# Kernel tuning notes

Hardware: AMD Instinct MI355X
Metric: run time of the kernel (lower is better)

The kernel has to match this reference:

```python
import jax, jax.numpy as jnp
import numpy as np
import math

D_HEAD = 64
EPS = 1e-6


def _rms_norm(x, scale, eps):
    # compute in float32 like the torch reference (promote_types with float32)
    xf = x.astype(jnp.float32)
    ms = jnp.mean(xf * xf, axis=-1, keepdims=True)
    return (xf * (scale.astype(jnp.float32) * jax.lax.rsqrt(ms + eps))).astype(x.dtype)


def _apply_rotary(x, cos, sin):
    # rotate first 2*cos_dim channels, pass the rest through
    ro = cos.shape[-1] * 2
    xr, xp = x[..., :ro], x[..., ro:]
    c = jnp.concatenate([cos, cos], axis=-1)
    s = jnp.concatenate([sin, sin], axis=-1)
    x1, x2 = jnp.split(xr, 2, axis=-1)
    rot = jnp.concatenate([-x2, x1], axis=-1)
    return jnp.concatenate([xr * c + rot * s, xp], axis=-1)


def _nb_idx(L, k):
    # NATTEN neighborhood start: window of size k clamped inside [0, L)
    i = jnp.arange(L)
    start = jnp.clip(i - k // 2, 0, L - k)
    return start[:, None] + jnp.arange(k)[None, :]  # [L, k]


def setup_inputs() -> dict:
    key = jax.random.key(0)
    ks = jax.random.split(key, 6)
    n, H, W, d_model, cond_features = 2, 48, 48, 256, 256
    x = jax.random.normal(ks[0], (n, H, W, d_model), dtype=jnp.float32)
    axis = jnp.linspace(-1.0, 1.0, H, dtype=jnp.float32)
    gh, gw = jnp.meshgrid(axis, axis, indexing='ij')
    pos = jnp.stack([gh, gw], axis=-1)  # [H, W, 2]
    cond = jax.random.normal(ks[1], (n, cond_features), dtype=jnp.float32)
    w_norm = jax.random.normal(ks[2], (d_model, cond_features), dtype=jnp.float32) * 0.01
    w_qkv = jax.random.normal(ks[3], (3 * d_model, d_model), dtype=jnp.float32) / math.sqrt(d_model)
    w_out = jax.random.normal(ks[4], (d_model, d_model), dtype=jnp.float32) * 0.02
    return {"x": x, "pos": pos, "cond": cond, "w_norm": w_norm, "w_qkv": w_qkv,
            "w_out": w_out, "kernel_size": 7}


def reference(x, pos, cond, w_norm, w_qkv, w_out, kernel_size):
    n, H, W, d_model = x.shape
    e = D_HEAD
    nh = d_model // e
    k = kernel_size
    skip = x

    # AdaRMSNorm: scale = linear(cond) + 1, broadcast over h, w
    scale = (cond @ w_norm.T)[:, None, None, :] + 1.0  # [n,1,1,d_model]
    xn = _rms_norm(x, scale, EPS)

    # QKV projection -> [3, n, nh, H, W, e]
    qkv = (xn @ w_qkv.T).reshape(n, H, W, 3, nh, e)
    qkv = jnp.transpose(qkv, (3, 0, 4, 1, 2, 5))
    q, kk, v = qkv[0], qkv[1], qkv[2]

    # Axial RoPE: freqs buffer of AxialRoPE(d_head // 2)
    dim = e // 2
    nf = dim // 4
    freqs = jnp.exp(jnp.linspace(math.log(math.pi), math.log(10.0 * math.pi), nf + 1)[:-1]).astype(jnp.float32)
    fh = pos[..., 0:1] * freqs  # [H,W,nf]
    fw = pos[..., 1:2] * freqs
    fr = jnp.concatenate([fh, fw], axis=-1)  # [H,W,2*nf] == [H,W,e//4]
    cos, sin = jnp.cos(fr), jnp.sin(fr)
    q = _apply_rotary(q, cos, sin)
    kk = _apply_rotary(kk, cos, sin)
    q = q / math.sqrt(e)

    # 2D neighborhood attention (natten2dqk / natten2dav, dilation 1)
    idx_h = _nb_idx(H, k)  # [H,k]
    idx_w = _nb_idx(W, k)  # [W,k]
    kg = kk[:, :, idx_h][:, :, :, :, idx_w]  # [n,nh,H,k,W,k,e]
    vg = v[:, :, idx_h][:, :, :, :, idx_w]   # [n,nh,H,k,W,k,e]
    qk = jnp.einsum('bmije,bmipjqe->bmijpq', q, kg).reshape(n, nh, H, W, k * k)
    a = jax.nn.softmax(qk, axis=-1).reshape(n, nh, H, W, k, k)
    o = jnp.einsum('bmijpq,bmipjqe->bmije', a, vg)  # [n,nh,H,W,e]

    o = jnp.transpose(o, (0, 2, 3, 1, 4)).reshape(n, H, W, d_model)
    return o @ w_out.T + skip
```

## Files before the change

### kernel.cpp

```cpp
#include <hip/hip_runtime.h>
#include <math.h>

#define N_B 2
#define HH 48
#define WW 48
#define DM 256
#define NH 4
#define EH 64
#define KS 7
#define NPIX (N_B*HH*WW)

typedef _Float16 half8 __attribute__((ext_vector_type(8)));
typedef _Float16 half4v __attribute__((ext_vector_type(4)));
typedef float float4v __attribute__((ext_vector_type(4)));

__global__ void scale_kernel(const float* __restrict__ cond,
                             const float* __restrict__ w_norm,
                             float* __restrict__ scale) {
    int b = blockIdx.x;
    int t = threadIdx.x, wave = t >> 6, lane = t & 63;
    int d = blockIdx.y*32 + wave*8 + (lane >> 3);
    int l8 = lane & 7;
    const float4* wr4 = (const float4*)(w_norm + (size_t)d*DM) + l8*8;
    const float4* c4  = (const float4*)(cond + (size_t)b*DM) + l8*8;
    float acc = 0.f;
    #pragma unroll
    for (int j = 0; j < 8; ++j) {
        float4 w = wr4[j], c = c4[j];
        acc += w.x*c.x + w.y*c.y + w.z*c.z + w.w*c.w;
    }
    acc += __shfl_xor(acc, 1, 64);
    acc += __shfl_xor(acc, 2, 64);
    acc += __shfl_xor(acc, 4, 64);
    if (l8 == 0) scale[b*DM + d] = acc + 1.0f;
}

__global__ __launch_bounds__(256) void gemm_qkv_fused(const float* __restrict__ x,
                                                      const float* __restrict__ scale,
                                                      const float* __restrict__ B,
                                                      const float* __restrict__ pos,
                                                      _Float16* __restrict__ qh,
                                                      _Float16* __restrict__ kh,
                                                      _Float16* __restrict__ vh) {
    const int LDA = 264, LDB = 40;
    __shared__ _Float16 As[64*LDA];
    __shared__ _Float16 Bs[2][128*LDB];
    int t = threadIdx.x;
    int wave = t >> 6, lane = t & 63;
    int m0 = blockIdx.x*64;
    int n0 = blockIdx.y*128;
    int b  = m0 / (HH*WW);

    {
        int tr = t >> 2, c4 = t & 3;
        const float4* xr = (const float4*)(x + (size_t)(m0 + tr)*DM);
        float4 xv[16];
        float ss = 0.f;
        #pragma unroll
        for (int j = 0; j < 16; ++j) {
            xv[j] = xr[c4 + j*4];
            ss += xv[j].x*xv[j].x + xv[j].y*xv[j].y + xv[j].z*xv[j].z + xv[j].w*xv[j].w;
        }
        ss += __shfl_xor(ss, 1, 64);
        ss += __shfl_xor(ss, 2, 64);
        float r = rsqrtf(ss*(1.0f/DM) + 1e-6f);
        const float* sc = scale + b*DM;
        #pragma unroll
        for (int j = 0; j < 16; ++j) {
            int c = (c4 + j*4)*4;
            float4 s4 = *(const float4*)(sc + c);
            half4v h;
            h[0] = (_Float16)(xv[j].x * s4.x * r);
            h[1] = (_Float16)(xv[j].y * s4.y * r);
            h[2] = (_Float16)(xv[j].z * s4.z * r);
            h[3] = (_Float16)(xv[j].w * s4.w * r);
            *(half4v*)&As[tr*LDA + c] = h;
        }
    }
    int br = t >> 1, kk = (t & 1)*16;
    {
        const float* bp = B + (size_t)(n0 + br)*DM + kk;
        float4 b0 = ((const float4*)bp)[0], b1 = ((const float4*)bp)[1];
        float4 b2 = ((const float4*)bp)[2], b3 = ((const float4*)bp)[3];
        half8 h0, h1;
        h0[0]=(_Float16)b0.x; h0[1]=(_Float16)b0.y; h0[2]=(_Float16)b0.z; h0[3]=(_Float16)b0.w;
        h0[4]=(_Float16)b1.x; h0[5]=(_Float16)b1.y; h0[6]=(_Float16)b1.z; h0[7]=(_Float16)b1.w;
        h1[0]=(_Float16)b2.x; h1[1]=(_Float16)b2.y; h1[2]=(_Float16)b2.z; h1[3]=(_Float16)b2.w;
        h1[4]=(_Float16)b3.x; h1[5]=(_Float16)b3.y; h1[6]=(_Float16)b3.z; h1[7]=(_Float16)b3.w;
        *(half8*)&Bs[0][br*LDB + kk]     = h0;
        *(half8*)&Bs[0][br*LDB + kk + 8] = h1;
    }
    __syncthreads();

    float4v acc[2][4];
    #pragma unroll
    for (int mi = 0; mi < 2; ++mi)
        #pragma unroll
        for (int ni = 0; ni < 4; ++ni) acc[mi][ni] = (float4v){0.f,0.f,0.f,0.f};

    int frow = lane & 15, kq = (lane >> 4)*8;
    int wm = wave >> 1, wn = wave & 1;

    for (int it = 0; it < 8; ++it) {
        int cur = it & 1;
        float4 nb0, nb1, nb2, nb3;
        if (it < 7) {
            const float* bp = B + (size_t)(n0 + br)*DM + (it + 1)*32 + kk;
            nb0 = ((const float4*)bp)[0]; nb1 = ((const float4*)bp)[1];
            nb2 = ((const float4*)bp)[2]; nb3 = ((const float4*)bp)[3];
        }
        int ka = it*32 + kq;
        half8 af0 = *(const half8*)&As[(wm*32 +  0 + frow)*LDA + ka];
        half8 af1 = *(const half8*)&As[(wm*32 + 16 + frow)*LDA + ka];
        #pragma unroll
        for (int ni = 0; ni < 4; ++ni) {
            half8 bf = *(const half8*)&Bs[cur][(wn*64 + ni*16 + frow)*LDB + kq];
            acc[0][ni] = __builtin_amdgcn_mfma_f32_16x16x32_f16(af0, bf, acc[0][ni], 0, 0, 0);
            acc[1][ni] = __builtin_amdgcn_mfma_f32_16x16x32_f16(af1, bf, acc[1][ni], 0, 0, 0);
        }
        if (it < 7) {
            half8 h0, h1;
            h0[0]=(_Float16)nb0.x; h0[1]=(_Float16)nb0.y; h0[2]=(_Float16)nb0.z; h0[3]=(_Float16)nb0.w;
            h0[4]=(_Float16)nb1.x; h0[5]=(_Float16)nb1.y; h0[6]=(_Float16)nb1.z; h0[7]=(_Float16)nb1.w;
            h1[0]=(_Float16)nb2.x; h1[1]=(_Float16)nb2.y; h1[2]=(_Float16)nb2.z; h1[3]=(_Float16)nb2.w;
            h1[4]=(_Float16)nb3.x; h1[5]=(_Float16)nb3.y; h1[6]=(_Float16)nb3.z; h1[7]=(_Float16)nb3.w;
            *(half8*)&Bs[cur^1][br*LDB + kk]     = h0;
            *(half8*)&Bs[cur^1][br*LDB + kk + 8] = h1;
            __syncthreads();
        }
    }

    int sel  = blockIdx.y >> 1;
    int head = (blockIdx.y & 1)*2 + wn;
    _Float16* outp = (sel == 0) ? qh : (sel == 1) ? kh : vh;
    int col = lane & 15, rbase = (lane >> 4)*4;
    float freq = __expf(1.14472988585f + (float)(col & 7) * 0.287823136624f);
    #pragma unroll
    for (int mi = 0; mi < 2; ++mi) {
        #pragma unroll
        for (int r = 0; r < 4; ++r) {
            int pix = m0 + wm*32 + mi*16 + rbase + r;
            float v0 = acc[mi][0][r], v1 = acc[mi][1][r], v2 = acc[mi][2][r], v3 = acc[mi][3][r];
            if (sel < 2) {
                int hw = pix % (HH*WW);
                float p = (col < 8) ? pos[hw*2] : pos[hw*2+1];
                float sn, cs;
                __sincosf(p*freq, &sn, &cs);
                float o0 = v0*cs - v1*sn;
                float o1 = v1*cs + v0*sn;
                v0 = o0; v1 = o1;
                if (sel == 0) { v0*=0.125f; v1*=0.125f; v2*=0.125f; v3*=0.125f; }
            }
            size_t base = (size_t)pix*DM + head*EH;
            outp[base +  0 + col] = (_Float16)v0;
            outp[base + 16 + col] = (_Float16)v1;
            outp[base + 32 + col] = (_Float16)v2;
            outp[base + 48 + col] = (_Float16)v3;
        }
    }
}

__global__ __launch_bounds__(256) void attn_mfma(const _Float16* __restrict__ qg,
                                                 const _Float16* __restrict__ kg,
                                                 const _Float16* __restrict__ vg,
                                                 _Float16* __restrict__ obuf) {
    __shared__ _Float16 VT[64*232];
    __shared__ _Float16 SP[64*232];
    int t = threadIdx.x;
    int wave = t >> 6, lane = t & 63;
    int col = lane & 15, quad = lane >> 4;
    int ty = blockIdx.x / 6, tx = blockIdx.x % 6;
    int b = blockIdx.y >> 2, head = blockIdx.y & 3;
    int qh0 = ty*8, qw0 = tx*8;
    int rh0 = min(max(qh0-3, 0), HH-14);
    int rw0 = min(max(qw0-3, 0), WW-14);

    {
        int nbl = t & 31;
        int e0  = (t >> 5) * 8;
        #pragma unroll
        for (int pass = 0; pass < 7; ++pass) {
            int nb = pass*32 + nbl;
            int nr = nb >> 4, nc = nb & 15;
            int pix = (b*HH + rh0+nr)*WW + rw0 + nc;
            half8 vv = *(const half8*)(vg + (size_t)pix*DM + head*EH + e0);
            #pragma unroll
            for (int i = 0; i < 8; ++i)
                VT[(e0+i)*232 + nb] = vv[i];
        }
    }

    int qidx_a = wave*16 + col;
    int pixq = (b*HH + qh0 + (qidx_a>>3))*WW + qw0 + (qidx_a & 7);
    const _Float16* qp = qg + (size_t)pixq*DM + head*EH;
    half8 qf0 = *(const half8*)(qp + quad*8);
    half8 qf1 = *(const half8*)(qp + 32 + quad*8);

    float4v s[14];
    #pragma unroll
    for (int nr = 0; nr < 14; ++nr) {
        int pixk = (b*HH + rh0+nr)*WW + rw0 + col;
        const _Float16* kp = kg + (size_t)pixk*DM + head*EH;
        half8 kf0 = *(const half8*)(kp + quad*8);
        half8 kf1 = *(const half8*)(kp + 32 + quad*8);
        float4v a = (float4v){0.f,0.f,0.f,0.f};
        a = __builtin_amdgcn_mfma_f32_16x16x32_f16(qf0, kf0, a, 0, 0, 0);
        a = __builtin_amdgcn_mfma_f32_16x16x32_f16(qf1, kf1, a, 0, 0, 0);
        s[nr] = a;
    }

    int sh_[4], uw_[4];
    #pragma unroll
    for (int r = 0; r < 4; ++r) {
        int qidx = wave*16 + quad*4 + r;
        int qhh = qh0 + (qidx>>3), qww = qw0 + (qidx & 7);
        sh_[r] = min(max(qhh-3, 0), HH-KS);
        int sw_ = min(max(qww-3, 0), WW-KS);
        uw_[r] = rw0 + col - sw_;
    }
    #pragma unroll
    for (int nr = 0; nr < 14; ++nr)
        #pragma unroll
        for (int r = 0; r < 4; ++r) {
            int uh = rh0 + nr - sh_[r];
            bool ok = ((unsigned)uh < 7u) && ((unsigned)uw_[r] < 7u);
            s[nr][r] = ok ? s[nr][r] : -1e30f;
        }
    #pragma unroll
    for (int r = 0; r < 4; ++r) {
        float m = s[0][r];
        #pragma unroll
        for (int nr = 1; nr < 14; ++nr) m = fmaxf(m, s[nr][r]);
        m = fmaxf(m, __shfl_xor(m, 1, 64));
        m = fmaxf(m, __shfl_xor(m, 2, 64));
        m = fmaxf(m, __shfl_xor(m, 4, 64));
        m = fmaxf(m, __shfl_xor(m, 8, 64));
        float sum = 0.f;
        #pragma unroll
        for (int nr = 0; nr < 14; ++nr) { float p = __expf(s[nr][r] - m); s[nr][r] = p; sum += p; }
        sum += __shfl_xor(sum, 1, 64);
        sum += __shfl_xor(sum, 2, 64);
        sum += __shfl_xor(sum, 4, 64);
        sum += __shfl_xor(sum, 8, 64);
        float rs = 1.f / sum;
        #pragma unroll
        for (int nr = 0; nr < 14; ++nr)
            SP[(wave*16 + quad*4 + r)*232 + nr*16 + col] = (_Float16)(s[nr][r] * rs);
    }
    __syncthreads();

    float4v o[4];
    #pragma unroll
    for (int dt = 0; dt < 4; ++dt) o[dt] = (float4v){0.f,0.f,0.f,0.f};
    #pragma unroll
    for (int ks = 0; ks < 7; ++ks) {
        half8 pa = *(const half8*)&SP[(wave*16 + col)*232 + ks*32 + quad*8];
        #pragma unroll
        for (int dt = 0; dt < 4; ++dt) {
            half8 vf = *(const half8*)&VT[(dt*16 + col)*232 + ks*32 + quad*8];
            o[dt] = __builtin_amdgcn_mfma_f32_16x16x32_f16(pa, vf, o[dt], 0, 0, 0);
        }
    }
    #pragma unroll
    for (int r = 0; r < 4; ++r) {
        int qidx = wave*16 + quad*4 + r;
        int pix = (b*HH + qh0 + (qidx>>3))*WW + qw0 + (qidx & 7);
        #pragma unroll
        for (int dt = 0; dt < 4; ++dt)
            obuf[(size_t)pix*DM + head*EH + dt*16 + col] = (_Float16)o[dt][r];
    }
}

__global__ __launch_bounds__(256) void gemm_out_f16(const _Float16* __restrict__ A,
                                                    const float* __restrict__ B,
                                                    float* __restrict__ C,
                                                    const float* __restrict__ skip) {
    const int LDA = 264, LDB = 40;
    __shared__ _Float16 As[64*LDA];
    __shared__ _Float16 Bs[2][64*LDB];
    int t = threadIdx.x;
    int wave = t >> 6, lane = t & 63;
    int m0 = blockIdx.x*64, n0 = blockIdx.y*64;

    {
        int tr = t >> 2, c8 = (t & 3)*8;
        const _Float16* ap = A + (size_t)(m0 + tr)*DM;
        #pragma unroll
        for (int j = 0; j < 8; ++j)
            *(half8*)&As[tr*LDA + c8 + j*32] = *(const half8*)(ap + c8 + j*32);
    }
    int br = t >> 2, kk = (t & 3)*8;
    {
        const float* bp = B + (size_t)(n0 + br)*DM + kk;
        float4 b0 = ((const float4*)bp)[0], b1 = ((const float4*)bp)[1];
        half8 h;
        h[0]=(_Float16)b0.x; h[1]=(_Float16)b0.y; h[2]=(_Float16)b0.z; h[3]=(_Float16)b0.w;
        h[4]=(_Float16)b1.x; h[5]=(_Float16)b1.y; h[6]=(_Float16)b1.z; h[7]=(_Float16)b1.w;
        *(half8*)&Bs[0][br*LDB + kk] = h;
    }
    __syncthreads();

    float4v acc[2][2];
    #pragma unroll
    for (int mi = 0; mi < 2; ++mi)
        #pragma unroll
        for (int ni = 0; ni < 2; ++ni) acc[mi][ni] = (float4v){0.f,0.f,0.f,0.f};

    int frow = lane & 15, kq = (lane >> 4)*8;
    int wm = wave >> 1, wn = wave & 1;

    for (int it = 0; it < 8; ++it) {
        int cur = it & 1;
        float4 nb0, nb1;
        if (it < 7) {
            const float* bp = B + (size_t)(n0 + br)*DM + (it + 1)*32 + kk;
            nb0 = ((const float4*)bp)[0]; nb1 = ((const float4*)bp)[1];
        }
        int ka = it*32 + kq;
        half8 af0 = *(const half8*)&As[(wm*32 +  0 + frow)*LDA + ka];
        half8 af1 = *(const half8*)&As[(wm*32 + 16 + frow)*LDA + ka];
        #pragma unroll
        for (int ni = 0; ni < 2; ++ni) {
            half8 bf = *(const half8*)&Bs[cur][(wn*32 + ni*16 + frow)*LDB + kq];
            acc[0][ni] = __builtin_amdgcn_mfma_f32_16x16x32_f16(af0, bf, acc[0][ni], 0, 0, 0);
            acc[1][ni] = __builtin_amdgcn_mfma_f32_16x16x32_f16(af1, bf, acc[1][ni], 0, 0, 0);
        }
        if (it < 7) {
            half8 h;
            h[0]=(_Float16)nb0.x; h[1]=(_Float16)nb0.y; h[2]=(_Float16)nb0.z; h[3]=(_Float16)nb0.w;
            h[4]=(_Float16)nb1.x; h[5]=(_Float16)nb1.y; h[6]=(_Float16)nb1.z; h[7]=(_Float16)nb1.w;
            *(half8*)&Bs[cur^1][br*LDB + kk] = h;
            __syncthreads();
        }
    }

    int col = lane & 15, rbase = (lane >> 4)*4;
    #pragma unroll
    for (int mi = 0; mi < 2; ++mi) {
        #pragma unroll
        for (int ni = 0; ni < 2; ++ni) {
            #pragma unroll
            for (int r = 0; r < 4; ++r) {
                int row = m0 + wm*32 + mi*16 + rbase + r;
                int c   = n0 + wn*32 + ni*16 + col;
                C[(size_t)row*DM + c] = acc[mi][ni][r] + skip[(size_t)row*DM + c];
            }
        }
    }
}

extern "C" void kernel_launch(void* const* d_in, const int* in_sizes, int n_in,
                              void* d_out, int out_size, void* d_ws, size_t ws_size,
                              hipStream_t stream) {
    const float* x      = (const float*)d_in[0];
    const float* pos    = (const float*)d_in[1];
    const float* cond   = (const float*)d_in[2];
    const float* w_norm = (const float*)d_in[3];
    const float* w_qkv  = (const float*)d_in[4];
    const float* w_out  = (const float*)d_in[5];
    float* out = (float*)d_out;
    char* base = (char*)d_ws;

    const size_t SZH = (size_t)NPIX*DM*2;
    const size_t PAD = 4096;
    float*    scale  = (float*)(base);
    _Float16* qh     = (_Float16*)(base + PAD);
    _Float16* kh     = (_Float16*)(base + PAD + 1*(SZH+PAD));
    _Float16* vh     = (_Float16*)(base + PAD + 2*(SZH+PAD));
    _Float16* obuf_h = (_Float16*)(base + PAD + 3*(SZH+PAD));

    scale_kernel<<<dim3(N_B, 8), 256, 0, stream>>>(cond, w_norm, scale);
    gemm_qkv_fused<<<dim3(NPIX/64, 6), 256, 0, stream>>>(x, scale, w_qkv, pos, qh, kh, vh);
    attn_mfma<<<dim3(36, N_B*NH), 256, 0, stream>>>(qh, kh, vh, obuf_h);
    gemm_out_f16<<<dim3(NPIX/64, DM/64), 256, 0, stream>>>(obuf_h, w_out, out, x);
}
```

Measured before the change: 105.8 us.

## Fuse all four kernels into one persistent cooperative kernel with grid syncs

Replaces the four separate launches (scale, QKV GEMM with norm and RoPE, neighborhood attention, output GEMM) with a single cooperative kernel of 256 blocks. Each stage loops over its former block indices as jobs and stages are separated by grid-wide syncs. The aim is to remove per-launch overhead and inter-kernel gaps. In exchange it adds grid barrier costs, shares one shared-memory buffer across stages, and caps parallelism at 256 blocks, so stages with more jobs than that (432 for QKV, 288 for attention and the output GEMM) run in several rounds.

```diff
diff --git a/kernel.cpp b/kernel.cpp
--- a/kernel.cpp
+++ b/kernel.cpp
@@ -1,5 +1,8 @@
 #include <hip/hip_runtime.h>
+#include <hip/hip_cooperative_groups.h>
 #include <math.h>
+
+namespace cg = cooperative_groups;
 
 #define N_B 2
 #define HH 48
@@ -9,341 +12,352 @@
 #define EH 64
 #define KS 7
 #define NPIX (N_B*HH*WW)
+#define GRID 256
 
 typedef _Float16 half8 __attribute__((ext_vector_type(8)));
 typedef _Float16 half4v __attribute__((ext_vector_type(4)));
 typedef float float4v __attribute__((ext_vector_type(4)));
 
-__global__ void scale_kernel(const float* __restrict__ cond,
-                             const float* __restrict__ w_norm,
-                             float* __restrict__ scale) {
-    int b = blockIdx.x;
-    int t = threadIdx.x, wave = t >> 6, lane = t & 63;
-    int d = blockIdx.y*32 + wave*8 + (lane >> 3);
-    int l8 = lane & 7;
-    const float4* wr4 = (const float4*)(w_norm + (size_t)d*DM) + l8*8;
-    const float4* c4  = (const float4*)(cond + (size_t)b*DM) + l8*8;
-    float acc = 0.f;
-    #pragma unroll
-    for (int j = 0; j < 8; ++j) {
-        float4 w = wr4[j], c = c4[j];
-        acc += w.x*c.x + w.y*c.y + w.z*c.z + w.w*c.w;
+__global__ __launch_bounds__(256) void fused_all(
+    const float* __restrict__ x,      const float* __restrict__ pos,
+    const float* __restrict__ cond,   const float* __restrict__ w_norm,
+    const float* __restrict__ w_qkv,  const float* __restrict__ w_out,
+    float* __restrict__ out,          float* __restrict__ scale,
+    _Float16* __restrict__ qh,        _Float16* __restrict__ kh,
+    _Float16* __restrict__ vh,        _Float16* __restrict__ obuf)
+{
+    __shared__ _Float16 SMEM[29696];
+    cg::grid_group grid = cg::this_grid();
+    const int bid = blockIdx.x;
+    const int t = threadIdx.x;
+    const int wave = t >> 6, lane = t & 63;
+
+    if (bid < 16) {
+        int b = bid >> 3;
+        int d = (bid & 7)*32 + wave*8 + (lane >> 3);
+        int l8 = lane & 7;
+        const float4* wr4 = (const float4*)(w_norm + (size_t)d*DM) + l8*8;
+        const float4* c4  = (const float4*)(cond + (size_t)b*DM) + l8*8;
+        float acc = 0.f;
+        #pragma unroll
+        for (int j = 0; j < 8; ++j) {
+            float4 w = wr4[j], c = c4[j];
+            acc += w.x*c.x + w.y*c.y + w.z*c.z + w.w*c.w;
+        }
+        acc += __shfl_xor(acc, 1, 64);
+        acc += __shfl_xor(acc, 2, 64);
+        acc += __shfl_xor(acc, 4, 64);
+        if (l8 == 0) scale[b*DM + d] = acc + 1.0f;
     }
-    acc += __shfl_xor(acc, 1, 64);
-    acc += __shfl_xor(acc, 2, 64);
-    acc += __shfl_xor(acc, 4, 64);
-    if (l8 == 0) scale[b*DM + d] = acc + 1.0f;
-}
-
-__global__ __launch_bounds__(256) void gemm_qkv_fused(const float* __restrict__ x,
-                                                      const float* __restrict__ scale,
-                                                      const float* __restrict__ B,
-                                                      const float* __restrict__ pos,
-                                                      _Float16* __restrict__ qh,
-                                                      _Float16* __restrict__ kh,
-                                                      _Float16* __restrict__ vh) {
-    const int LDA = 264, LDB = 40;
-    __shared__ _Float16 As[64*LDA];
-    __shared__ _Float16 Bs[2][128*LDB];
-    int t = threadIdx.x;
-    int wave = t >> 6, lane = t & 63;
-    int m0 = blockIdx.x*64;
-    int n0 = blockIdx.y*128;
-    int b  = m0 / (HH*WW);
+    __threadfence();
+    grid.sync();
 
     {
-        int tr = t >> 2, c4 = t & 3;
-        const float4* xr = (const float4*)(x + (size_t)(m0 + tr)*DM);
-        float4 xv[16];
-        float ss = 0.f;
-        #pragma unroll
-        for (int j = 0; j < 16; ++j) {
-            xv[j] = xr[c4 + j*4];
-            ss += xv[j].x*xv[j].x + xv[j].y*xv[j].y + xv[j].z*xv[j].z + xv[j].w*xv[j].w;
-        }
-        ss += __shfl_xor(ss, 1, 64);
-        ss += __shfl_xor(ss, 2, 64);
-        float r = rsqrtf(ss*(1.0f/DM) + 1e-6f);
-        const float* sc = scale + b*DM;
-        #pragma unroll
-        for (int j = 0; j < 16; ++j) {
-            int c = (c4 + j*4)*4;
-            float4 s4 = *(const float4*)(sc + c);
-            half4v h;
-            h[0] = (_Float16)(xv[j].x * s4.x * r);
-            h[1] = (_Float16)(xv[j].y * s4.y * r);
-            h[2] = (_Float16)(xv[j].z * s4.z * r);
-            h[3] = (_Float16)(xv[j].w * s4.w * r);
-            *(half4v*)&As[tr*LDA + c] = h;
+        const int LDA = 264, LDB = 40;
+        _Float16* As  = SMEM;
+        _Float16* Bs0 = SMEM + 16896;
+        _Float16* Bs1 = SMEM + 22016;
+        const int frow = lane & 15, kq = (lane >> 4)*8;
+        const int wm = wave >> 1, wn = wave & 1;
+        for (int job = bid; job < 432; job += GRID) {
+            const int bx = job % 72, by = job / 72;
+            const int m0 = bx*64, n0 = by*128;
+            const int b  = m0 / (HH*WW);
+            __syncthreads();
+            {
+                int tr = t >> 2, c4i = t & 3;
+                const float4* xr = (const float4*)(x + (size_t)(m0 + tr)*DM);
+                float4 xv[16];
+                float ss = 0.f;
+                #pragma unroll
+                for (int j = 0; j < 16; ++j) {
+                    xv[j] = xr[c4i + j*4];
+                    ss += xv[j].x*xv[j].x + xv[j].y*xv[j].y + xv[j].z*xv[j].z + xv[j].w*xv[j].w;
+                }
+                ss += __shfl_xor(ss, 1, 64);
+                ss += __shfl_xor(ss, 2, 64);
+                float r = rsqrtf(ss*(1.0f/DM) + 1e-6f);
+                const float* sc = scale + b*DM;
+                #pragma unroll
+                for (int j = 0; j < 16; ++j) {
+                    int c = (c4i + j*4)*4;
+                    float4 s4 = *(const float4*)(sc + c);
+                    half4v h;
+                    h[0] = (_Float16)(xv[j].x * s4.x * r);
+                    h[1] = (_Float16)(xv[j].y * s4.y * r);
+                    h[2] = (_Float16)(xv[j].z * s4.z * r);
+                    h[3] = (_Float16)(xv[j].w * s4.w * r);
+                    *(half4v*)&As[tr*LDA + c] = h;
+                }
+            }
+            int br = t >> 1, kk = (t & 1)*16;
+            {
+                const float* bp = w_qkv + (size_t)(n0 + br)*DM + kk;
+                float4 b0 = ((const float4*)bp)[0], b1 = ((const float4*)bp)[1];
+                float4 b2 = ((const float4*)bp)[2], b3 = ((const float4*)bp)[3];
+                half8 h0, h1;
+                h0[0]=(_Float16)b0.x; h0[1]=(_Float16)b0.y; h0[2]=(_Float16)b0.z; h0[3]=(_Float16)b0.w;
+                h0[4]=(_Float16)b1.x; h0[5]=(_Float16)b1.y; h0[6]=(_Float16)b1.z; h0[7]=(_Float16)b1.w;
+                h1[0]=(_Float16)b2.x; h1[1]=(_Float16)b2.y; h1[2]=(_Float16)b2.z; h1[3]=(_Float16)b2.w;
+                h1[4]=(_Float16)b3.x; h1[5]=(_Float16)b3.y; h1[6]=(_Float16)b3.z; h1[7]=(_Float16)b3.w;
+                *(half8*)&Bs0[br*LDB + kk]     = h0;
+                *(half8*)&Bs0[br*LDB + kk + 8] = h1;
+            }
+            __syncthreads();
+
+            float4v acc[2][4];
+            #pragma unroll
+            for (int mi = 0; mi < 2; ++mi)
+                #pragma unroll
+                for (int ni = 0; ni < 4; ++ni) acc[mi][ni] = (float4v){0.f,0.f,0.f,0.f};
+
+            for (int it = 0; it < 8; ++it) {
+                _Float16* Bc = (it & 1) ? Bs1 : Bs0;
+                _Float16* Bn = (it & 1) ? Bs0 : Bs1;
+                float4 nb0, nb1, nb2, nb3;
+                if (it < 7) {
+                    const float* bp = w_qkv + (size_t)(n0 + br)*DM + (it + 1)*32 + kk;
+                    nb0 = ((const float4*)bp)[0]; nb1 = ((const float4*)bp)[1];
+                    nb2 = ((const float4*)bp)[2]; nb3 = ((const float4*)bp)[3];
+                }
+                int ka = it*32 + kq;
+                half8 af0 = *(const half8*)&As[(wm*32 +  0 + frow)*LDA + ka];
+                half8 af1 = *(const half8*)&As[(wm*32 + 16 + frow)*LDA + ka];
+                #pragma unroll
+                for (int ni = 0; ni < 4; ++ni) {
+                    half8 bf = *(const half8*)&Bc[(wn*64 + ni*16 + frow)*LDB + kq];
+                    acc[0][ni] = __builtin_amdgcn_mfma_f32_16x16x32_f16(af0, bf, acc[0][ni], 0, 0, 0);
+                    acc[1][ni] = __builtin_amdgcn_mfma_f32_16x16x32_f16(af1, bf, acc[1][ni], 0, 0, 0);
+                }
+                if (it < 7) {
+                    half8 h0, h1;
+                    h0[0]=(_Float16)nb0.x; h0[1]=(_Float16)nb0.y; h0[2]=(_Float16)nb0.z; h0[3]=(_Float16)nb0.w;
+                    h0[4]=(_Float16)nb1.x; h0[5]=(_Float16)nb1.y; h0[6]=(_Float16)nb1.z; h0[7]=(_Float16)nb1.w;
+                    h1[0]=(_Float16)nb2.x; h1[1]=(_Float16)nb2.y; h1[2]=(_Float16)nb2.z; h1[3]=(_Float16)nb2.w;
+                    h1[4]=(_Float16)nb3.x; h1[5]=(_Float16)nb3.y; h1[6]=(_Float16)nb3.z; h1[7]=(_Float16)nb3.w;
+                    *(half8*)&Bn[br*LDB + kk]     = h0;
+                    *(half8*)&Bn[br*LDB + kk + 8] = h1;
+                    __syncthreads();
+                }
+            }
+
+            int sel  = by >> 1;
+            int head = (by & 1)*2 + wn;
+            _Float16* outp = (sel == 0) ? qh : (sel == 1) ? kh : vh;
+            int col = lane & 15, rbase = (lane >> 4)*4;
+            float freq = __expf(1.14472988585f + (float)(col & 7) * 0.287823136624f);
+            #pragma unroll
+            for (int mi = 0; mi < 2; ++mi) {
+                #pragma unroll
+                for (int r = 0; r < 4; ++r) {
+                    int pix = m0 + wm*32 + mi*16 + rbase + r;
+                    float v0 = acc[mi][0][r], v1 = acc[mi][1][r], v2 = acc[mi][2][r], v3 = acc[mi][3][r];
+                    if (sel < 2) {
+                        int hw = pix % (HH*WW);
+                        float p = (col < 8) ? pos[hw*2] : pos[hw*2+1];
+                        float sn, cs;
+                        __sincosf(p*freq, &sn, &cs);
+                        float o0 = v0*cs - v1*sn;
+                        float o1 = v1*cs + v0*sn;
+                        v0 = o0; v1 = o1;
+                        if (sel == 0) { v0*=0.125f; v1*=0.125f; v2*=0.125f; v3*=0.125f; }
+                    }
+                    size_t base = (size_t)pix*DM + head*EH;
+                    outp[base +  0 + col] = (_Float16)v0;
+                    outp[base + 16 + col] = (_Float16)v1;
+                    outp[base + 32 + col] = (_Float16)v2;
+                    outp[base + 48 + col] = (_Float16)v3;
+                }
+            }
         }
     }
-    int br = t >> 1, kk = (t & 1)*16;
+    __threadfence();
+    grid.sync();
+
     {
-        const float* bp = B + (size_t)(n0 + br)*DM + kk;
-        float4 b0 = ((const float4*)bp)[0], b1 = ((const float4*)bp)[1];
-        float4 b2 = ((const float4*)bp)[2], b3 = ((const float4*)bp)[3];
-        half8 h0, h1;
-        h0[0]=(_Float16)b0.x; h0[1]=(_Float16)b0.y; h0[2]=(_Float16)b0.z; h0[3]=(_Float16)b0.w;
-        h0[4]=(_Float16)b1.x; h0[5]=(_Float16)b1.y; h0[6]=(_Float16)b1.z; h0[7]=(_Float16)b1.w;
-        h1[0]=(_Float16)b2.x; h1[1]=(_Float16)b2.y; h1[2]=(_Float16)b2.z; h1[3]=(_Float16)b2.w;
-        h1[4]=(_Float16)b3.x; h1[5]=(_Float16)b3.y; h1[6]=(_Float16)b3.z; h1[7]=(_Float16)b3.w;
-        *(half8*)&Bs[0][br*LDB + kk]     = h0;
-        *(half8*)&Bs[0][br*LDB + kk + 8] = h1;
-    }
-    __syncthreads();
-
-    float4v acc[2][4];
-    #pragma unroll
-    for (int mi = 0; mi < 2; ++mi)
-        #pragma unroll
-        for (int ni = 0; ni < 4; ++ni) acc[mi][ni] = (float4v){0.f,0.f,0.f,0.f};
-
-    int frow = lane & 15, kq = (lane >> 4)*8;
-    int wm = wave >> 1, wn = wave & 1;
-
-    for (int it = 0; it < 8; ++it) {
-        int cur = it & 1;
-        float4 nb0, nb1, nb2, nb3;
-        if (it < 7) {
-            const float* bp = B + (size_t)(n0 + br)*DM + (it + 1)*32 + kk;
-            nb0 = ((const float4*)bp)[0]; nb1 = ((const float4*)bp)[1];
-            nb2 = ((const float4*)bp)[2]; nb3 = ((const float4*)bp)[3];
-        }
-        int ka = it*32 + kq;
-        half8 af0 = *(const half8*)&As[(wm*32 +  0 + frow)*LDA + ka];
-        half8 af1 = *(const half8*)&As[(wm*32 + 16 + frow)*LDA + ka];
-        #pragma unroll
-        for (int ni = 0; ni < 4; ++ni) {
-            half8 bf = *(const half8*)&Bs[cur][(wn*64 + ni*16 + frow)*LDB + kq];
-            acc[0][ni] = __builtin_amdgcn_mfma_f32_16x16x32_f16(af0, bf, acc[0][ni], 0, 0, 0);
-            acc[1][ni] = __builtin_amdgcn_mfma_f32_16x16x32_f16(af1, bf, acc[1][ni], 0, 0, 0);
-        }
-        if (it < 7) {
-            half8 h0, h1;
-            h0[0]=(_Float16)nb0.x; h0[1]=(_Float16)nb0.y; h0[2]=(_Float16)nb0.z; h0[3]=(_Float16)nb0.w;
-            h0[4]=(_Float16)nb1.x; h0[5]=(_Float16)nb1.y; h0[6]=(_Float16)nb1.z; h0[7]=(_Float16)nb1.w;
-            h1[0]=(_Float16)nb2.x; h1[1]=(_Float16)nb2.y; h1[2]=(_Float16)nb2.z; h1[3]=(_Float16)nb2.w;
-            h1[4]=(_Float16)nb3.x; h1[5]=(_Float16)nb3.y; h1[6]=(_Float16)nb3.z; h1[7]=(_Float16)nb3.w;
-            *(half8*)&Bs[cur^1][br*LDB + kk]     = h0;
-            *(half8*)&Bs[cur^1][br*LDB + kk + 8] = h1;
-            __syncthreads();
+        _Float16* VT = SMEM;
+        _Float16* SP = SMEM + 14848;
+        const int col = lane & 15, quad = lane >> 4;
+        for (int job = bid; job < 288; job += GRID) {
+            int gx = job % 36, gy = job / 36;
+            int ty = gx / 6, tx = gx % 6;
+            int b = gy >> 2, head = gy & 3;
+            int qh0 = ty*8, qw0 = tx*8;
+            int rh0 = min(max(qh0-3, 0), HH-14);
+            int rw0 = min(max(qw0-3, 0), WW-14);
+            __syncthreads();
+            {
+                int nbl = t & 31;
+                int e0  = (t >> 5) * 8;
+                #pragma unroll
+                for (int pass = 0; pass < 7; ++pass) {
+                    int nb = pass*32 + nbl;
+                    int nr = nb >> 4, nc = nb & 15;
+                    int pix = (b*HH + rh0+nr)*WW + rw0 + nc;
+                    half8 vv = *(const half8*)(vh + (size_t)pix*DM + head*EH + e0);
+                    #pragma unroll
+                    for (int i = 0; i < 8; ++i)
+                        VT[(e0+i)*232 + nb] = vv[i];
+                }
+            }
+
+            int qidx_a = wave*16 + col;
+            int pixq = (b*HH + qh0 + (qidx_a>>3))*WW + qw0 + (qidx_a & 7);
+            const _Float16* qp = qh + (size_t)pixq*DM + head*EH;
+            half8 qf0 = *(const half8*)(qp + quad*8);
+            half8 qf1 = *(const half8*)(qp + 32 + quad*8);
+
+            float4v s[14];
+            #pragma unroll
+            for (int nr = 0; nr < 14; ++nr) {
+                int pixk = (b*HH + rh0+nr)*WW + rw0 + col;
+                const _Float16* kp = kh + (size_t)pixk*DM + head*EH;
+                half8 kf0 = *(const half8*)(kp + quad*8);
+                half8 kf1 = *(const half8*)(kp + 32 + quad*8);
+                float4v a = (float4v){0.f,0.f,0.f,0.f};
+                a = __builtin_amdgcn_mfma_f32_16x16x32_f16(qf0, kf0, a, 0, 0, 0);
+                a = __builtin_amdgcn_mfma_f32_16x16x32_f16(qf1, kf1, a, 0, 0, 0);
+                s[nr] = a;
+            }
+
+            int sh_[4], uw_[4];
+            #pragma unroll
+            for (int r = 0; r < 4; ++r) {
+                int qidx = wave*16 + quad*4 + r;
+                int qhh = qh0 + (qidx>>3), qww = qw0 + (qidx & 7);
+                sh_[r] = min(max(qhh-3, 0), HH-KS);
+                int sw_ = min(max(qww-3, 0), WW-KS);
+                uw_[r] = rw0 + col - sw_;
+            }
+            #pragma unroll
+            for (int nr = 0; nr < 14; ++nr)
+                #pragma unroll
+                for (int r = 0; r < 4; ++r) {
+                    int uh = rh0 + nr - sh_[r];
+                    bool ok = ((unsigned)uh < 7u) && ((unsigned)uw_[r] < 7u);
+                    s[nr][r] = ok ? s[nr][r] : -1e30f;
+                }
+            #pragma unroll
+            for (int r = 0; r < 4; ++r) {
+                float m = s[0][r];
+                #pragma unroll
+                for (int nr = 1; nr < 14; ++nr) m = fmaxf(m, s[nr][r]);
+                m = fmaxf(m, __shfl_xor(m, 1, 64));
+                m = fmaxf(m, __shfl_xor(m, 2, 64));
+                m = fmaxf(m, __shfl_xor(m, 4, 64));
+                m = fmaxf(m, __shfl_xor(m, 8, 64));
+                float sum = 0.f;
+                #pragma unroll
+                for (int nr = 0; nr < 14; ++nr) { float p = __expf(s[nr][r] - m); s[nr][r] = p; sum += p; }
+                sum += __shfl_xor(sum, 1, 64);
+                sum += __shfl_xor(sum, 2, 64);
+                sum += __shfl_xor(sum, 4, 64);
+                sum += __shfl_xor(sum, 8, 64);
+                float rs = 1.f / sum;
+                #pragma unroll
+                for (int nr = 0; nr < 14; ++nr)
+                    SP[(wave*16 + quad*4 + r)*232 + nr*16 + col] = (_Float16)(s[nr][r] * rs);
+            }
+            __syncthreads();
+
+            float4v o[4];
+            #pragma unroll
+            for (int dt = 0; dt < 4; ++dt) o[dt] = (float4v){0.f,0.f,0.f,0.f};
+            #pragma unroll
+            for (int ks = 0; ks < 7; ++ks) {
+                half8 pa = *(const half8*)&SP[(wave*16 + col)*232 + ks*32 + quad*8];
+                #pragma unroll
+                for (int dt = 0; dt < 4; ++dt) {
+                    half8 vf = *(const half8*)&VT[(dt*16 + col)*232 + ks*32 + quad*8];
+                    o[dt] = __builtin_amdgcn_mfma_f32_16x16x32_f16(pa, vf, o[dt], 0, 0, 0);
+                }
+            }
+            #pragma unroll
+            for (int r = 0; r < 4; ++r) {
+                int qidx = wave*16 + quad*4 + r;
+                int pix = (b*HH + qh0 + (qidx>>3))*WW + qw0 + (qidx & 7);
+                #pragma unroll
+                for (int dt = 0; dt < 4; ++dt)
+                    obuf[(size_t)pix*DM + head*EH + dt*16 + col] = (_Float16)o[dt][r];
+            }
         }
     }
-
-    int sel  = blockIdx.y >> 1;
-    int head = (blockIdx.y & 1)*2 + wn;
-    _Float16* outp = (sel == 0) ? qh : (sel == 1) ? kh : vh;
-    int col = lane & 15, rbase = (lane >> 4)*4;
-    float freq = __expf(1.14472988585f + (float)(col & 7) * 0.287823136624f);
-    #pragma unroll
-    for (int mi = 0; mi < 2; ++mi) {
-        #pragma unroll
-        for (int r = 0; r < 4; ++r) {
-            int pix = m0 + wm*32 + mi*16 + rbase + r;
-            float v0 = acc[mi][0][r], v1 = acc[mi][1][r], v2 = acc[mi][2][r], v3 = acc[mi][3][r];
-            if (sel < 2) {
-                int hw = pix % (HH*WW);
-                float p = (col < 8) ? pos[hw*2] : pos[hw*2+1];
-                float sn, cs;
-                __sincosf(p*freq, &sn, &cs);
-                float o0 = v0*cs - v1*sn;
-                float o1 = v1*cs + v0*sn;
-                v0 = o0; v1 = o1;
-                if (sel == 0) { v0*=0.125f; v1*=0.125f; v2*=0.125f; v3*=0.125f; }
-            }
-            size_t base = (size_t)pix*DM + head*EH;
-            outp[base +  0 + col] = (_Float16)v0;
-            outp[base + 16 + col] = (_Float16)v1;
-            outp[base + 32 + col] = (_Float16)v2;
-            outp[base + 48 + col] = (_Float16)v3;
-        }
-    }
-}
-
-__global__ __launch_bounds__(256) void attn_mfma(const _Float16* __restrict__ qg,
-                                                 const _Float16* __restrict__ kg,
-                                                 const _Float16* __restrict__ vg,
-                                                 _Float16* __restrict__ obuf) {
-    __shared__ _Float16 VT[64*232];
-    __shared__ _Float16 SP[64*232];
-    int t = threadIdx.x;
-    int wave = t >> 6, lane = t & 63;
-    int col = lane & 15, quad = lane >> 4;
-    int ty = blockIdx.x / 6, tx = blockIdx.x % 6;
-    int b = blockIdx.y >> 2, head = blockIdx.y & 3;
-    int qh0 = ty*8, qw0 = tx*8;
-    int rh0 = min(max(qh0-3, 0), HH-14);
-    int rw0 = min(max(qw0-3, 0), WW-14);
+    __threadfence();
+    grid.sync();
 
     {
-        int nbl = t & 31;
-        int e0  = (t >> 5) * 8;
-        #pragma unroll
-        for (int pass = 0; pass < 7; ++pass) {
-            int nb = pass*32 + nbl;
-            int nr = nb >> 4, nc = nb & 15;
-            int pix = (b*HH + rh0+nr)*WW + rw0 + nc;
-            half8 vv = *(const half8*)(vg + (size_t)pix*DM + head*EH + e0);
-            #pragma unroll
-            for (int i = 0; i < 8; ++i)
-                VT[(e0+i)*232 + nb] = vv[i];
-        }
-    }
-
-    int qidx_a = wave*16 + col;
-    int pixq = (b*HH + qh0 + (qidx_a>>3))*WW + qw0 + (qidx_a & 7);
-    const _Float16* qp = qg + (size_t)pixq*DM + head*EH;
-    half8 qf0 = *(const half8*)(qp + quad*8);
-    half8 qf1 = *(const half8*)(qp + 32 + quad*8);
-
-    float4v s[14];
-    #pragma unroll
-    for (int nr = 0; nr < 14; ++nr) {
-        int pixk = (b*HH + rh0+nr)*WW + rw0 + col;
-        const _Float16* kp = kg + (size_t)pixk*DM + head*EH;
-        half8 kf0 = *(const half8*)(kp + quad*8);
-        half8 kf1 = *(const half8*)(kp + 32 + quad*8);
-        float4v a = (float4v){0.f,0.f,0.f,0.f};
-        a = __builtin_amdgcn_mfma_f32_16x16x32_f16(qf0, kf0, a, 0, 0, 0);
-        a = __builtin_amdgcn_mfma_f32_16x16x32_f16(qf1, kf1, a, 0, 0, 0);
-        s[nr] = a;
-    }
-
-    int sh_[4], uw_[4];
-    #pragma unroll
-    for (int r = 0; r < 4; ++r) {
-        int qidx = wave*16 + quad*4 + r;
-        int qhh = qh0 + (qidx>>3), qww = qw0 + (qidx & 7);
-        sh_[r] = min(max(qhh-3, 0), HH-KS);
-        int sw_ = min(max(qww-3, 0), WW-KS);
-        uw_[r] = rw0 + col - sw_;
-    }
-    #pragma unroll
-    for (int nr = 0; nr < 14; ++nr)
-        #pragma unroll
-        for (int r = 0; r < 4; ++r) {
-            int uh = rh0 + nr - sh_[r];
-            bool ok = ((unsigned)uh < 7u) && ((unsigned)uw_[r] < 7u);
-            s[nr][r] = ok ? s[nr][r] : -1e30f;
-        }
-    #pragma unroll
-    for (int r = 0; r < 4; ++r) {
-        float m = s[0][r];
-        #pragma unroll
-        for (int nr = 1; nr < 14; ++nr) m = fmaxf(m, s[nr][r]);
-        m = fmaxf(m, __shfl_xor(m, 1, 64));
-        m = fmaxf(m, __shfl_xor(m, 2, 64));
-        m = fmaxf(m, __shfl_xor(m, 4, 64));
-        m = fmaxf(m, __shfl_xor(m, 8, 64));
-        float sum = 0.f;
-        #pragma unroll
-        for (int nr = 0; nr < 14; ++nr) { float p = __expf(s[nr][r] - m); s[nr][r] = p; sum += p; }
-        sum += __shfl_xor(sum, 1, 64);
-        sum += __shfl_xor(sum, 2, 64);
-        sum += __shfl_xor(sum, 4, 64);
-        sum += __shfl_xor(sum, 8, 64);
-        float rs = 1.f / sum;
-        #pragma unroll
-        for (int nr = 0; nr < 14; ++nr)
-            SP[(wave*16 + quad*4 + r)*232 + nr*16 + col] = (_Float16)(s[nr][r] * rs);
-    }
-    __syncthreads();
-
-    float4v o[4];
-    #pragma unroll
-    for (int dt = 0; dt < 4; ++dt) o[dt] = (float4v){0.f,0.f,0.f,0.f};
-    #pragma unroll
-    for (int ks = 0; ks < 7; ++ks) {
-        half8 pa = *(const half8*)&SP[(wave*16 + col)*232 + ks*32 + quad*8];
-        #pragma unroll
-        for (int dt = 0; dt < 4; ++dt) {
-            half8 vf = *(const half8*)&VT[(dt*16 + col)*232 + ks*32 + quad*8];
-            o[dt] = __builtin_amdgcn_mfma_f32_16x16x32_f16(pa, vf, o[dt], 0, 0, 0);
-        }
-    }
-    #pragma unroll
-    for (int r = 0; r < 4; ++r) {
-        int qidx = wave*16 + quad*4 + r;
-        int pix = (b*HH + qh0 + (qidx>>3))*WW + qw0 + (qidx & 7);
-        #pragma unroll
-        for (int dt = 0; dt < 4; ++dt)
-            obuf[(size_t)pix*DM + head*EH + dt*16 + col] = (_Float16)o[dt][r];
-    }
-}
-
-__global__ __launch_bounds__(256) void gemm_out_f16(const _Float16* __restrict__ A,
-                                                    const float* __restrict__ B,
-                                                    float* __restrict__ C,
-                                                    const float* __restrict__ skip) {
-    const int LDA = 264, LDB = 40;
-    __shared__ _Float16 As[64*LDA];
-    __shared__ _Float16 Bs[2][64*LDB];
-    int t = threadIdx.x;
-    int wave = t >> 6, lane = t & 63;
-    int m0 = blockIdx.x*64, n0 = blockIdx.y*64;
-
-    {
-        int tr = t >> 2, c8 = (t & 3)*8;
-        const _Float16* ap = A + (size_t)(m0 + tr)*DM;
-        #pragma unroll
-        for (int j = 0; j < 8; ++j)
-            *(half8*)&As[tr*LDA + c8 + j*32] = *(const half8*)(ap + c8 + j*32);
-    }
-    int br = t >> 2, kk = (t & 3)*8;
-    {
-        const float* bp = B + (size_t)(n0 + br)*DM + kk;
-        float4 b0 = ((const float4*)bp)[0], b1 = ((const float4*)bp)[1];
-        half8 h;
-        h[0]=(_Float16)b0.x; h[1]=(_Float16)b0.y; h[2]=(_Float16)b0.z; h[3]=(_Float16)b0.w;
-        h[4]=(_Float16)b1.x; h[5]=(_Float16)b1.y; h[6]=(_Float16)b1.z; h[7]=(_Float16)b1.w;
-        *(half8*)&Bs[0][br*LDB + kk] = h;
-    }
-    __syncthreads();
-
-    float4v acc[2][2];
-    #pragma unroll
-    for (int mi = 0; mi < 2; ++mi)
-        #pragma unroll
-        for (int ni = 0; ni < 2; ++ni) acc[mi][ni] = (float4v){0.f,0.f,0.f,0.f};
-
-    int frow = lane & 15, kq = (lane >> 4)*8;
-    int wm = wave >> 1, wn = wave & 1;
-
-    for (int it = 0; it < 8; ++it) {
-        int cur = it & 1;
-        float4 nb0, nb1;
-        if (it < 7) {
-            const float* bp = B + (size_t)(n0 + br)*DM + (it + 1)*32 + kk;
-            nb0 = ((const float4*)bp)[0]; nb1 = ((const float4*)bp)[1];
-        }
-        int ka = it*32 + kq;
-        half8 af0 = *(const half8*)&As[(wm*32 +  0 + frow)*LDA + ka];
-        half8 af1 = *(const half8*)&As[(wm*32 + 16 + frow)*LDA + ka];
-        #pragma unroll
-        for (int ni = 0; ni < 2; ++ni) {
-            half8 bf = *(const half8*)&Bs[cur][(wn*32 + ni*16 + frow)*LDB + kq];
-            acc[0][ni] = __builtin_amdgcn_mfma_f32_16x16x32_f16(af0, bf, acc[0][ni], 0, 0, 0);
-            acc[1][ni] = __builtin_amdgcn_mfma_f32_16x16x32_f16(af1, bf, acc[1][ni], 0, 0, 0);
-        }
-        if (it < 7) {
-            half8 h;
-            h[0]=(_Float16)nb0.x; h[1]=(_Float16)nb0.y; h[2]=(_Float16)nb0.z; h[3]=(_Float16)nb0.w;
-            h[4]=(_Float16)nb1.x; h[5]=(_Float16)nb1.y; h[6]=(_Float16)nb1.z; h[7]=(_Float16)nb1.w;
-            *(half8*)&Bs[cur^1][br*LDB + kk] = h;
-            __syncthreads();
-        }
-    }
-
-    int col = lane & 15, rbase = (lane >> 4)*4;
-    #pragma unroll
-    for (int mi = 0; mi < 2; ++mi) {
-        #pragma unroll
-        for (int ni = 0; ni < 2; ++ni) {
-            #pragma unroll
-            for (int r = 0; r < 4; ++r) {
-                int row = m0 + wm*32 + mi*16 + rbase + r;
-                int c   = n0 + wn*32 + ni*16 + col;
-                C[(size_t)row*DM + c] = acc[mi][ni][r] + skip[(size_t)row*DM + c];
+        const int LDA = 264, LDB = 40;
+        _Float16* As  = SMEM;
+        _Float16* Bs0 = SMEM + 16896;
+        _Float16* Bs1 = SMEM + 19456;
+        const int frow = lane & 15, kq = (lane >> 4)*8;
+        const int wm = wave >> 1, wn = wave & 1;
+        for (int job = bid; job < 288; job += GRID) {
+            int bx = job % 72, by = job / 72;
+            int m0 = bx*64, n0 = by*64;
+            __syncthreads();
+            {
+                int tr = t >> 2, c8 = (t & 3)*8;
+                const _Float16* ap = obuf + (size_t)(m0 + tr)*DM;
+                #pragma unroll
+                for (int j = 0; j < 8; ++j)
+                    *(half8*)&As[tr*LDA + c8 + j*32] = *(const half8*)(ap + c8 + j*32);
+            }
+            int br = t >> 2, kk = (t & 3)*8;
+            {
+                const float* bp = w_out + (size_t)(n0 + br)*DM + kk;
+                float4 b0 = ((const float4*)bp)[0], b1 = ((const float4*)bp)[1];
+                half8 h;
+                h[0]=(_Float16)b0.x; h[1]=(_Float16)b0.y; h[2]=(_Float16)b0.z; h[3]=(_Float16)b0.w;
+                h[4]=(_Float16)b1.x; h[5]=(_Float16)b1.y; h[6]=(_Float16)b1.z; h[7]=(_Float16)b1.w;
+                *(half8*)&Bs0[br*LDB + kk] = h;
+            }
+            __syncthreads();
+
+            float4v acc[2][2];
+            #pragma unroll
+            for (int mi = 0; mi < 2; ++mi)
+                #pragma unroll
+                for (int ni = 0; ni < 2; ++ni) acc[mi][ni] = (float4v){0.f,0.f,0.f,0.f};
+
+            for (int it = 0; it < 8; ++it) {
+                _Float16* Bc = (it & 1) ? Bs1 : Bs0;
+                _Float16* Bn = (it & 1) ? Bs0 : Bs1;
+                float4 nb0, nb1;
+                if (it < 7) {
+                    const float* bp = w_out + (size_t)(n0 + br)*DM + (it + 1)*32 + kk;
+                    nb0 = ((const float4*)bp)[0]; nb1 = ((const float4*)bp)[1];
+                }
+                int ka = it*32 + kq;
+                half8 af0 = *(const half8*)&As[(wm*32 +  0 + frow)*LDA + ka];
+                half8 af1 = *(const half8*)&As[(wm*32 + 16 + frow)*LDA + ka];
+                #pragma unroll
+                for (int ni = 0; ni < 2; ++ni) {
+                    half8 bf = *(const half8*)&Bc[(wn*32 + ni*16 + frow)*LDB + kq];
+                    acc[0][ni] = __builtin_amdgcn_mfma_f32_16x16x32_f16(af0, bf, acc[0][ni], 0, 0, 0);
+                    acc[1][ni] = __builtin_amdgcn_mfma_f32_16x16x32_f16(af1, bf, acc[1][ni], 0, 0, 0);
+                }
+                if (it < 7) {
+                    half8 h;
+                    h[0]=(_Float16)nb0.x; h[1]=(_Float16)nb0.y; h[2]=(_Float16)nb0.z; h[3]=(_Float16)nb0.w;
+                    h[4]=(_Float16)nb1.x; h[5]=(_Float16)nb1.y; h[6]=(_Float16)nb1.z; h[7]=(_Float16)nb1.w;
+                    *(half8*)&Bn[br*LDB + kk] = h;
+                    __syncthreads();
+                }
+            }
+
+            int col = lane & 15, rbase = (lane >> 4)*4;
+            #pragma unroll
+            for (int mi = 0; mi < 2; ++mi) {
+                #pragma unroll
+                for (int ni = 0; ni < 2; ++ni) {
+                    #pragma unroll
+                    for (int r = 0; r < 4; ++r) {
+                        int row = m0 + wm*32 + mi*16 + rbase + r;
+                        int c   = n0 + wn*32 + ni*16 + col;
+                        out[(size_t)row*DM + c] = acc[mi][ni][r] + x[(size_t)row*DM + c];
+                    }
+                }
             }
         }
     }
@@ -367,10 +381,13 @@
     _Float16* qh     = (_Float16*)(base + PAD);
     _Float16* kh     = (_Float16*)(base + PAD + 1*(SZH+PAD));
     _Float16* vh     = (_Float16*)(base + PAD + 2*(SZH+PAD));
-    _Float16* obuf_h = (_Float16*)(base + PAD + 3*(SZH+PAD));
-
-    scale_kernel<<<dim3(N_B, 8), 256, 0, stream>>>(cond, w_norm, scale);
-    gemm_qkv_fused<<<dim3(NPIX/64, 6), 256, 0, stream>>>(x, scale, w_qkv, pos, qh, kh, vh);
-    attn_mfma<<<dim3(36, N_B*NH), 256, 0, stream>>>(qh, kh, vh, obuf_h);
-    gemm_out_f16<<<dim3(NPIX/64, DM/64), 256, 0, stream>>>(obuf_h, w_out, out, x);
+    _Float16* obuf   = (_Float16*)(base + PAD + 3*(SZH+PAD));
+
+    void* args[] = {
+        (void*)&x, (void*)&pos, (void*)&cond, (void*)&w_norm,
+        (void*)&w_qkv, (void*)&w_out, (void*)&out, (void*)&scale,
+        (void*)&qh, (void*)&kh, (void*)&vh, (void*)&obuf
+    };
+    hipLaunchCooperativeKernel((const void*)fused_all, dim3(GRID), dim3(256),
+                               args, 0, stream);
 }
```

New measurement: 271.7 us. 2.57x slower.
